# Kernel tuning notes

Hardware: AMD Instinct MI355X
Metric: run time of the kernel (lower is better)

Reference implementation:

```python
import jax, jax.numpy as jnp
import numpy as np

N_ROWS = 4096   # output dim (c_3)
N_COLS = 4096   # input dim (c_4)
NNZ = 4194304


def setup_inputs() -> dict:
    key = jax.random.key(0)
    k1, k2, k3, k4 = jax.random.split(key, 4)
    x = jax.random.normal(k1, (4, 2048, N_COLS), dtype=jnp.float32)
    values = jax.random.normal(k2, (NNZ,), dtype=jnp.float32)
    col_idx = jax.random.randint(k3, (NNZ,), 0, N_COLS, dtype=jnp.int32)
    row_ids = jnp.sort(jax.random.randint(k4, (NNZ,), 0, N_ROWS, dtype=jnp.int32))
    return {"x": x, "values": values, "col_idx": col_idx, "row_ids": row_ids}


def reference(x, values, col_idx, row_ids):
    # Faithful math of macko_spmv.multiply applied to every flattened row of x:
    #   out[..., r] = sum_k values[k] * x[..., col_idx[k]]  where row_ids[k] == r
    # Instead of N separate sparse matvecs (the original Python loop), scatter the
    # compressed weights into the dense matrix once and do a single batched GEMM.
    W = jnp.zeros((N_ROWS, N_COLS), dtype=values.dtype).at[row_ids, col_idx].add(values)
    return jnp.einsum('bsh,oh->bso', x, W)  # [B, S, N_ROWS]
```

## Files before the change

### kernel.cpp

```cpp
#include <hip/hip_runtime.h>


#define M_DIM 8192
#define K_DIM 4096
#define N_DIM 4096
#define NNZ   4194304
#define FXSCALE 1048576.0f
#define FXINV  (1.0f / 1048576.0f)

#define BKT 64
#define NTIL (K_DIM / BKT)
#define ABUF 16384

typedef __bf16 bf16x8 __attribute__((ext_vector_type(8)));
typedef float  floatx4 __attribute__((ext_vector_type(4)));
typedef unsigned short ushort8 __attribute__((ext_vector_type(8)));

__device__ __forceinline__ unsigned short f32_to_bf16(float f) {
  unsigned int u = __float_as_uint(f);
  u += 0x7FFFu + ((u >> 16) & 1u);
  return (unsigned short)(u >> 16);
}

__device__ __forceinline__ void async_copy16(const void* g, void* l) {
  __builtin_amdgcn_global_load_lds(
      (const __attribute__((address_space(1))) void*)g,
      (__attribute__((address_space(3))) void*)l,
      16, 0, 0);
}

__global__ void row_start_kernel(const int* __restrict__ rows,
                                 int* __restrict__ row_start) {
  int i = blockIdx.x * blockDim.x + threadIdx.x;
  if (i > NNZ) return;
  int cur  = (i < NNZ) ? rows[i] : N_DIM;
  int prev = (i > 0) ? rows[i - 1] : -1;
  for (int r = prev + 1; r <= cur; ++r) row_start[r] = i;
}

__global__ __launch_bounds__(256) void build_w_kernel(
    const float* __restrict__ vals,
    const int* __restrict__ cols,
    const int* __restrict__ row_start,
    unsigned short* __restrict__ Wb) {
  __shared__ int wrow[K_DIM];

  const int r = blockIdx.x;
  for (int i = threadIdx.x; i < K_DIM; i += 256) wrow[i] = 0;
  __syncthreads();

  const int start = row_start[r];
  const int end   = row_start[r + 1];
  for (int i = start + threadIdx.x; i < end; i += 256)
    atomicAdd(&wrow[cols[i]], (int)lrintf(vals[i] * FXSCALE));
  __syncthreads();

  ushort8* dst = (ushort8*)(Wb + (size_t)r * K_DIM);
  for (int i = threadIdx.x; i < K_DIM / 8; i += 256) {
    const int* s = &wrow[i * 8];
    ushort8 o;
#pragma unroll
    for (int j = 0; j < 8; j++) o[j] = f32_to_bf16((float)s[j] * FXINV);
    dst[i] = o;
  }
}

__global__ void cvt_kernel(const float4* __restrict__ in,
                           ushort4* __restrict__ out, int n4) {
  int i = blockIdx.x * blockDim.x + threadIdx.x;
  if (i < n4) {
    float4 v = in[i];
    ushort4 o;
    o.x = f32_to_bf16(v.x);
    o.y = f32_to_bf16(v.y);
    o.z = f32_to_bf16(v.z);
    o.w = f32_to_bf16(v.w);
    out[i] = o;
  }
}

#define BAR()   asm volatile("s_barrier" ::: "memory")
#define LGKM0() do { asm volatile("s_waitcnt lgkmcnt(0)" ::: "memory"); \
                     __builtin_amdgcn_sched_barrier(0); } while (0)
#define VMW6()  asm volatile("s_waitcnt vmcnt(6)" ::: "memory")
#define VMW0()  asm volatile("s_waitcnt vmcnt(0)" ::: "memory")

#define STAGEH(Gb_, Lb_, h_, kt_) do {                                          \
  async_copy16((Gb_) + (size_t)((h_)*128 +      srow) * K_DIM + (kt_),          \
               (Lb_) + (h_)*8192 +        tid * 8);                             \
  async_copy16((Gb_) + (size_t)((h_)*128 + 64 + srow) * K_DIM + (kt_),          \
               (Lb_) + (h_)*8192 + 4096 + tid * 8);                             \
} while (0)

#define RD_A(Ab_, mb_) do {                                                     \
  _Pragma("unroll")                                                             \
  for (int m_ = 0; m_ < 4; ++m_) {                                              \
    af[m_][0] = *(const bf16x8*)((Ab_) + offA[(mb_) + m_][0]);                  \
    af[m_][1] = *(const bf16x8*)((Ab_) + offA[(mb_) + m_][1]);                  \
  }                                                                             \
} while (0)

#define RD_B(Bb_, nb_) do {                                                     \
  _Pragma("unroll")                                                             \
  for (int n_ = 0; n_ < 2; ++n_) {                                              \
    bf[(nb_) + n_][0] = *(const bf16x8*)((Bb_) + offB[(nb_) + n_][0]);          \
    bf[(nb_) + n_][1] = *(const bf16x8*)((Bb_) + offB[(nb_) + n_][1]);          \
  }                                                                             \
} while (0)

#define MM(mb_, nb_) do {                                                       \
  __builtin_amdgcn_s_setprio(1);                                                \
  _Pragma("unroll")                                                             \
  for (int m_ = 0; m_ < 4; ++m_)                                                \
    _Pragma("unroll")                                                           \
    for (int n_ = 0; n_ < 2; ++n_) {                                            \
      acc[(mb_) + m_][(nb_) + n_] = __builtin_amdgcn_mfma_f32_16x16x32_bf16(    \
          af[m_][0], bf[(nb_) + n_][0], acc[(mb_) + m_][(nb_) + n_], 0, 0, 0);  \
      acc[(mb_) + m_][(nb_) + n_] = __builtin_amdgcn_mfma_f32_16x16x32_bf16(    \
          af[m_][1], bf[(nb_) + n_][1], acc[(mb_) + m_][(nb_) + n_], 0, 0, 0);  \
    }                                                                           \
  __builtin_amdgcn_s_setprio(0);                                                \
} while (0)

__global__ __launch_bounds__(512, 2) void gemm_bt(
    const unsigned short* __restrict__ A,
    const unsigned short* __restrict__ B,
    float* __restrict__ C) {
  __shared__ __attribute__((aligned(16))) unsigned short LDS[4][ABUF];

  const int tid  = threadIdx.x;
  const int wid  = tid >> 6;
  const int lane = tid & 63;
  const int quad = lane >> 4;
  const int l16  = lane & 15;
  const int mh   = wid >> 2;
  const int w32  = wid & 3;

  int wg = blockIdx.x;
  wg = (wg & 7) * 64 + (wg >> 3);
  const int n0 = (wg & 15) * 256;
  const int m0 = (wg >> 4) * 256;

  const int srow = tid >> 3;
  const int sblk = ((tid & 7) ^ ((tid >> 3) & 7)) * 8;
  const unsigned short* Abase = A + (size_t)m0 * K_DIM + sblk;
  const unsigned short* Bbase = B + (size_t)n0 * K_DIM + sblk;

  int offA[8][2], offB[4][2];
#pragma unroll
  for (int m = 0; m < 8; ++m) {
    const int r = (m < 4 ? mh * 64 + m * 16 : 128 + mh * 64 + (m - 4) * 16) + l16;
#pragma unroll
    for (int h = 0; h < 2; ++h)
      offA[m][h] = r * 64 + (((h * 4 + quad) ^ (r & 7)) * 8);
  }
#pragma unroll
  for (int n = 0; n < 4; ++n) {
    const int r = (n < 2 ? w32 * 32 + n * 16 : 128 + w32 * 32 + (n - 2) * 16) + l16;
#pragma unroll
    for (int h = 0; h < 2; ++h)
      offB[n][h] = r * 64 + (((h * 4 + quad) ^ (r & 7)) * 8);
  }

  floatx4 acc[8][4];
#pragma unroll
  for (int i = 0; i < 8; i++)
#pragma unroll
    for (int j = 0; j < 4; j++) acc[i][j] = (floatx4){0.f, 0.f, 0.f, 0.f};

  bf16x8 af[4][2], bf[4][2];

  unsigned short* A0L = &LDS[0][0];
  unsigned short* B0L = &LDS[1][0];
  unsigned short* A1L = &LDS[2][0];
  unsigned short* B1L = &LDS[3][0];

  STAGEH(Abase, A0L, 0, 0);
  STAGEH(Bbase, B0L, 0, 0);
  STAGEH(Abase, A0L, 1, 0);
  STAGEH(Bbase, B0L, 1, 0);
  STAGEH(Abase, A1L, 0, BKT);
  STAGEH(Bbase, B1L, 0, BKT);
  STAGEH(Abase, A1L, 1, BKT);
  VMW6();
  BAR();

  for (int i = 0; i < NTIL / 2 - 1; ++i) {
    const int ktE = (2 * i) * BKT;
    RD_A(A0L, 0); RD_B(B0L, 0);
    STAGEH(Bbase, B1L, 1, ktE + BKT);
    BAR(); LGKM0();
    MM(0, 0);
    BAR();
    RD_B(B0L, 2);
    STAGEH(Abase, A0L, 0, ktE + 2 * BKT);
    BAR(); LGKM0();
    MM(0, 2);
    BAR();
    RD_A(A0L, 4);
    STAGEH(Bbase, B0L, 0, ktE + 2 * BKT);
    BAR(); LGKM0();
    MM(4, 0);
    BAR();
    STAGEH(Abase, A0L, 1, ktE + 2 * BKT);
    BAR();
    MM(4, 2);
    VMW6();
    BAR();
    RD_A(A1L, 0); RD_B(B1L, 0);
    STAGEH(Bbase, B0L, 1, ktE + 2 * BKT);
    BAR(); LGKM0();
    MM(0, 0);
    BAR();
    RD_B(B1L, 2);
    STAGEH(Abase, A1L, 0, ktE + 3 * BKT);
    BAR(); LGKM0();
    MM(0, 2);
    BAR();
    RD_A(A1L, 4);
    STAGEH(Bbase, B1L, 0, ktE + 3 * BKT);
    BAR(); LGKM0();
    MM(4, 0);
    BAR();
    STAGEH(Abase, A1L, 1, ktE + 3 * BKT);
    BAR();
    MM(4, 2);
    VMW6();
    BAR();
  }

  {
    const int ktE = (NTIL - 2) * BKT;
    RD_A(A0L, 0); RD_B(B0L, 0);
    STAGEH(Bbase, B1L, 1, ktE + BKT);
    BAR(); LGKM0();
    MM(0, 0);
    BAR();
    RD_B(B0L, 2);
    BAR(); LGKM0();
    MM(0, 2);
    BAR();
    RD_A(A0L, 4);
    BAR(); LGKM0();
    MM(4, 0);
    BAR();
    MM(4, 2);
    VMW0();
    BAR();
    RD_A(A1L, 0); RD_B(B1L, 0);
    BAR(); LGKM0();
    MM(0, 0);
    BAR();
    RD_B(B1L, 2);
    BAR(); LGKM0();
    MM(0, 2);
    BAR();
    RD_A(A1L, 4);
    BAR(); LGKM0();
    MM(4, 0);
    BAR();
    MM(4, 2);
  }

#pragma unroll
  for (int m = 0; m < 8; m++) {
    const int mrow = (m < 4 ? mh * 64 + m * 16 : 128 + mh * 64 + (m - 4) * 16);
#pragma unroll
    for (int r = 0; r < 4; r++) {
      const int row = m0 + mrow + quad * 4 + r;
      float* Cp = C + (size_t)row * N_DIM + n0 + l16;
#pragma unroll
      for (int n = 0; n < 4; n++) {
        const int ncol = (n < 2 ? w32 * 32 + n * 16 : 128 + w32 * 32 + (n - 2) * 16);
        Cp[ncol] = acc[m][n][r];
      }
    }
  }
}

extern "C" void kernel_launch(void* const* d_in, const int* in_sizes, int n_in,
                              void* d_out, int out_size, void* d_ws, size_t ws_size,
                              hipStream_t stream) {
  const float* x       = (const float*)d_in[0];
  const float* values  = (const float*)d_in[1];
  const int*   col_idx = (const int*)d_in[2];
  const int*   row_ids = (const int*)d_in[3];
  float* out = (float*)d_out;

  unsigned short* Wb = (unsigned short*)d_ws;
  unsigned short* Xb = (unsigned short*)((char*)d_ws + ((size_t)32 << 20));
  int* row_start     = (int*)((char*)d_ws + ((size_t)96 << 20));

  const int x4 = M_DIM * K_DIM / 4;

  row_start_kernel<<<(NNZ + 256) / 256, 256, 0, stream>>>(row_ids, row_start);
  cvt_kernel<<<(x4 + 255) / 256, 256, 0, stream>>>((const float4*)x, (ushort4*)Xb, x4);
  build_w_kernel<<<N_DIM, 256, 0, stream>>>(values, col_idx, row_start, Wb);

  gemm_bt<<<dim3(512), 512, 0, stream>>>(Xb, Wb, out);
}
```

Before: 466.9 us.

## Fuse preprocessing kernels into one launch and precompute LDS read pointers

Replaces the row_start, conversion and weight-build kernels with a single preprocessing kernel. Each weight-row block finds its row range by binary search over the sorted row ids, and the remaining blocks convert x to bf16 with a grid-stride loop. This removes two launches, the row_start pass and its global buffer, and lets the conversion overlap with the weight build. In the GEMM, the per-fragment LDS offset arrays are replaced by eight base pointers plus compile-time constant offsets, which should lower register pressure and address arithmetic. The cost is two binary searches of about 22 steps per weight block.

```diff
diff --git a/kernel.cpp b/kernel.cpp
--- a/kernel.cpp
+++ b/kernel.cpp
@@ -11,6 +11,7 @@
 #define BKT 64
 #define NTIL (K_DIM / BKT)
 #define ABUF 16384
+#define CVT_BLOCKS 8192
 
 typedef __bf16 bf16x8 __attribute__((ext_vector_type(8)));
 typedef float  floatx4 __attribute__((ext_vector_type(4)));
@@ -29,53 +30,48 @@
       16, 0, 0);
 }
 
-__global__ void row_start_kernel(const int* __restrict__ rows,
-                                 int* __restrict__ row_start) {
-  int i = blockIdx.x * blockDim.x + threadIdx.x;
-  if (i > NNZ) return;
-  int cur  = (i < NNZ) ? rows[i] : N_DIM;
-  int prev = (i > 0) ? rows[i - 1] : -1;
-  for (int r = prev + 1; r <= cur; ++r) row_start[r] = i;
-}
-
-__global__ __launch_bounds__(256) void build_w_kernel(
-    const float* __restrict__ vals,
-    const int* __restrict__ cols,
-    const int* __restrict__ row_start,
-    unsigned short* __restrict__ Wb) {
-  __shared__ int wrow[K_DIM];
-
-  const int r = blockIdx.x;
-  for (int i = threadIdx.x; i < K_DIM; i += 256) wrow[i] = 0;
-  __syncthreads();
-
-  const int start = row_start[r];
-  const int end   = row_start[r + 1];
-  for (int i = start + threadIdx.x; i < end; i += 256)
-    atomicAdd(&wrow[cols[i]], (int)lrintf(vals[i] * FXSCALE));
-  __syncthreads();
-
-  ushort8* dst = (ushort8*)(Wb + (size_t)r * K_DIM);
-  for (int i = threadIdx.x; i < K_DIM / 8; i += 256) {
-    const int* s = &wrow[i * 8];
-    ushort8 o;
-#pragma unroll
-    for (int j = 0; j < 8; j++) o[j] = f32_to_bf16((float)s[j] * FXINV);
-    dst[i] = o;
-  }
-}
-
-__global__ void cvt_kernel(const float4* __restrict__ in,
-                           ushort4* __restrict__ out, int n4) {
-  int i = blockIdx.x * blockDim.x + threadIdx.x;
-  if (i < n4) {
-    float4 v = in[i];
-    ushort4 o;
-    o.x = f32_to_bf16(v.x);
-    o.y = f32_to_bf16(v.y);
-    o.z = f32_to_bf16(v.z);
-    o.w = f32_to_bf16(v.w);
-    out[i] = o;
+__global__ __launch_bounds__(256) void preproc_kernel(
+    const float4* __restrict__ x4in, ushort4* __restrict__ xbout,
+    const float* __restrict__ vals, const int* __restrict__ cols,
+    const int* __restrict__ rows, unsigned short* __restrict__ Wb) {
+  if (blockIdx.x < N_DIM) {
+    __shared__ int wrow[K_DIM];
+    const int r = blockIdx.x;
+
+    int lo = 0, hi = NNZ;
+    while (lo < hi) { int mid = (lo + hi) >> 1; if (rows[mid] < r) lo = mid + 1; else hi = mid; }
+    const int start = lo;
+    hi = NNZ;
+    while (lo < hi) { int mid = (lo + hi) >> 1; if (rows[mid] < r + 1) lo = mid + 1; else hi = mid; }
+    const int end = lo;
+
+    for (int i = threadIdx.x; i < K_DIM; i += 256) wrow[i] = 0;
+    __syncthreads();
+
+    for (int i = start + threadIdx.x; i < end; i += 256)
+      atomicAdd(&wrow[cols[i]], (int)lrintf(vals[i] * FXSCALE));
+    __syncthreads();
+
+    ushort8* dst = (ushort8*)(Wb + (size_t)r * K_DIM);
+    for (int i = threadIdx.x; i < K_DIM / 8; i += 256) {
+      const int* s = &wrow[i * 8];
+      ushort8 o;
+#pragma unroll
+      for (int j = 0; j < 8; j++) o[j] = f32_to_bf16((float)s[j] * FXINV);
+      dst[i] = o;
+    }
+  } else {
+    const int total = M_DIM * K_DIM / 4;
+    for (int i = (blockIdx.x - N_DIM) * 256 + threadIdx.x; i < total;
+         i += CVT_BLOCKS * 256) {
+      float4 v = x4in[i];
+      ushort4 o;
+      o.x = f32_to_bf16(v.x);
+      o.y = f32_to_bf16(v.y);
+      o.z = f32_to_bf16(v.z);
+      o.w = f32_to_bf16(v.w);
+      xbout[i] = o;
+    }
   }
 }
 
@@ -92,19 +88,22 @@
                (Lb_) + (h_)*8192 + 4096 + tid * 8);                             \
 } while (0)
 
-#define RD_A(Ab_, mb_) do {                                                     \
+#define ROFA(m_) ((m_) < 4 ? (m_) * 1024 : 8192 + ((m_) - 4) * 1024)
+#define ROFB(n_) ((n_) < 2 ? (n_) * 1024 : 8192 + ((n_) - 2) * 1024)
+
+#define RD_A(p0_, p1_, mb_) do {                                                \
   _Pragma("unroll")                                                             \
   for (int m_ = 0; m_ < 4; ++m_) {                                              \
-    af[m_][0] = *(const bf16x8*)((Ab_) + offA[(mb_) + m_][0]);                  \
-    af[m_][1] = *(const bf16x8*)((Ab_) + offA[(mb_) + m_][1]);                  \
+    af[m_][0] = *(const bf16x8*)((p0_) + ROFA((mb_) + m_));                     \
+    af[m_][1] = *(const bf16x8*)((p1_) + ROFA((mb_) + m_));                     \
   }                                                                             \
 } while (0)
 
-#define RD_B(Bb_, nb_) do {                                                     \
+#define RD_B(p0_, p1_, nb_) do {                                                \
   _Pragma("unroll")                                                             \
   for (int n_ = 0; n_ < 2; ++n_) {                                              \
-    bf[(nb_) + n_][0] = *(const bf16x8*)((Bb_) + offB[(nb_) + n_][0]);          \
-    bf[(nb_) + n_][1] = *(const bf16x8*)((Bb_) + offB[(nb_) + n_][1]);          \
+    bf[(nb_) + n_][0] = *(const bf16x8*)((p0_) + ROFB((nb_) + n_));             \
+    bf[(nb_) + n_][1] = *(const bf16x8*)((p1_) + ROFB((nb_) + n_));             \
   }                                                                             \
 } while (0)
 
@@ -146,21 +145,20 @@
   const unsigned short* Abase = A + (size_t)m0 * K_DIM + sblk;
   const unsigned short* Bbase = B + (size_t)n0 * K_DIM + sblk;
 
-  int offA[8][2], offB[4][2];
-#pragma unroll
-  for (int m = 0; m < 8; ++m) {
-    const int r = (m < 4 ? mh * 64 + m * 16 : 128 + mh * 64 + (m - 4) * 16) + l16;
-#pragma unroll
-    for (int h = 0; h < 2; ++h)
-      offA[m][h] = r * 64 + (((h * 4 + quad) ^ (r & 7)) * 8);
-  }
-#pragma unroll
-  for (int n = 0; n < 4; ++n) {
-    const int r = (n < 2 ? w32 * 32 + n * 16 : 128 + w32 * 32 + (n - 2) * 16) + l16;
-#pragma unroll
-    for (int h = 0; h < 2; ++h)
-      offB[n][h] = r * 64 + (((h * 4 + quad) ^ (r & 7)) * 8);
-  }
+  const int r7  = l16 & 7;
+  const int xt0 = (quad ^ r7) * 8;
+  const int xt1 = ((4 + quad) ^ r7) * 8;
+  const int aB  = (mh * 64 + l16) * 64;
+  const int bB  = (w32 * 32 + l16) * 64;
+
+  const unsigned short* pA0h0 = &LDS[0][0] + aB + xt0;
+  const unsigned short* pA0h1 = &LDS[0][0] + aB + xt1;
+  const unsigned short* pB0h0 = &LDS[1][0] + bB + xt0;
+  const unsigned short* pB0h1 = &LDS[1][0] + bB + xt1;
+  const unsigned short* pA1h0 = &LDS[2][0] + aB + xt0;
+  const unsigned short* pA1h1 = &LDS[2][0] + aB + xt1;
+  const unsigned short* pB1h0 = &LDS[3][0] + bB + xt0;
+  const unsigned short* pB1h1 = &LDS[3][0] + bB + xt1;
 
   floatx4 acc[8][4];
 #pragma unroll
@@ -187,17 +185,17 @@
 
   for (int i = 0; i < NTIL / 2 - 1; ++i) {
     const int ktE = (2 * i) * BKT;
-    RD_A(A0L, 0); RD_B(B0L, 0);
+    RD_A(pA0h0, pA0h1, 0); RD_B(pB0h0, pB0h1, 0);
     STAGEH(Bbase, B1L, 1, ktE + BKT);
     BAR(); LGKM0();
     MM(0, 0);
     BAR();
-    RD_B(B0L, 2);
+    RD_B(pB0h0, pB0h1, 2);
     STAGEH(Abase, A0L, 0, ktE + 2 * BKT);
     BAR(); LGKM0();
     MM(0, 2);
     BAR();
-    RD_A(A0L, 4);
+    RD_A(pA0h0, pA0h1, 4);
     STAGEH(Bbase, B0L, 0, ktE + 2 * BKT);
     BAR(); LGKM0();
     MM(4, 0);
@@ -207,17 +205,17 @@
     MM(4, 2);
     VMW6();
     BAR();
-    RD_A(A1L, 0); RD_B(B1L, 0);
+    RD_A(pA1h0, pA1h1, 0); RD_B(pB1h0, pB1h1, 0);
     STAGEH(Bbase, B0L, 1, ktE + 2 * BKT);
     BAR(); LGKM0();
     MM(0, 0);
     BAR();
-    RD_B(B1L, 2);
+    RD_B(pB1h0, pB1h1, 2);
     STAGEH(Abase, A1L, 0, ktE + 3 * BKT);
     BAR(); LGKM0();
     MM(0, 2);
     BAR();
-    RD_A(A1L, 4);
+    RD_A(pA1h0, pA1h1, 4);
     STAGEH(Bbase, B1L, 0, ktE + 3 * BKT);
     BAR(); LGKM0();
     MM(4, 0);
@@ -231,31 +229,31 @@
 
   {
     const int ktE = (NTIL - 2) * BKT;
-    RD_A(A0L, 0); RD_B(B0L, 0);
+    RD_A(pA0h0, pA0h1, 0); RD_B(pB0h0, pB0h1, 0);
     STAGEH(Bbase, B1L, 1, ktE + BKT);
     BAR(); LGKM0();
     MM(0, 0);
     BAR();
-    RD_B(B0L, 2);
-    BAR(); LGKM0();
-    MM(0, 2);
-    BAR();
-    RD_A(A0L, 4);
+    RD_B(pB0h0, pB0h1, 2);
+    BAR(); LGKM0();
+    MM(0, 2);
+    BAR();
+    RD_A(pA0h0, pA0h1, 4);
     BAR(); LGKM0();
     MM(4, 0);
     BAR();
     MM(4, 2);
     VMW0();
     BAR();
-    RD_A(A1L, 0); RD_B(B1L, 0);
-    BAR(); LGKM0();
-    MM(0, 0);
-    BAR();
-    RD_B(B1L, 2);
-    BAR(); LGKM0();
-    MM(0, 2);
-    BAR();
-    RD_A(A1L, 4);
+    RD_A(pA1h0, pA1h1, 0); RD_B(pB1h0, pB1h1, 0);
+    BAR(); LGKM0();
+    MM(0, 0);
+    BAR();
+    RD_B(pB1h0, pB1h1, 2);
+    BAR(); LGKM0();
+    MM(0, 2);
+    BAR();
+    RD_A(pA1h0, pA1h1, 4);
     BAR(); LGKM0();
     MM(4, 0);
     BAR();
@@ -289,13 +287,9 @@
 
   unsigned short* Wb = (unsigned short*)d_ws;
   unsigned short* Xb = (unsigned short*)((char*)d_ws + ((size_t)32 << 20));
-  int* row_start     = (int*)((char*)d_ws + ((size_t)96 << 20));
-
-  const int x4 = M_DIM * K_DIM / 4;
-
-  row_start_kernel<<<(NNZ + 256) / 256, 256, 0, stream>>>(row_ids, row_start);
-  cvt_kernel<<<(x4 + 255) / 256, 256, 0, stream>>>((const float4*)x, (ushort4*)Xb, x4);
-  build_w_kernel<<<N_DIM, 256, 0, stream>>>(values, col_idx, row_start, Wb);
+
+  preproc_kernel<<<N_DIM + CVT_BLOCKS, 256, 0, stream>>>(
+      (const float4*)x, (ushort4*)Xb, values, col_idx, row_ids, Wb);
 
   gemm_bt<<<dim3(512), 512, 0, stream>>>(Xb, Wb, out);
 }
```

New measurement: 481.5 us. +3.1%, slower.

## Switch GEMM inner loop from 16x16x32 to 32x32x16 bf16 MFMA tiles

Applied to the files above, without the earlier changes.

Replaces the 16x16x32 MFMA micro-tiles with 32x32x16 MFMA instructions, which reorganizes the accumulator layout (4x2 floatx16 instead of 8x4 floatx4), the LDS fragment reads and the epilogue store mapping. It also reorders the LDS buffers to A0,A1,B0,B1 so fragment pointers can be precomputed once and indexed by constant offsets instead of per-fragment offset tables. The larger MFMA shape is meant to cut LDS read traffic per FLOP and instruction-issue overhead. In exchange, the epilogue store pattern changes and register pressure shifts.

```diff
diff --git a/kernel.cpp b/kernel.cpp
--- a/kernel.cpp
+++ b/kernel.cpp
@@ -13,7 +13,7 @@
 #define ABUF 16384
 
 typedef __bf16 bf16x8 __attribute__((ext_vector_type(8)));
-typedef float  floatx4 __attribute__((ext_vector_type(4)));
+typedef float  floatx16 __attribute__((ext_vector_type(16)));
 typedef unsigned short ushort8 __attribute__((ext_vector_type(8)));
 
 __device__ __forceinline__ unsigned short f32_to_bf16(float f) {
@@ -92,33 +92,36 @@
                (Lb_) + (h_)*8192 + 4096 + tid * 8);                             \
 } while (0)
 
-#define RD_A(Ab_, mb_) do {                                                     \
-  _Pragma("unroll")                                                             \
-  for (int m_ = 0; m_ < 4; ++m_) {                                              \
-    af[m_][0] = *(const bf16x8*)((Ab_) + offA[(mb_) + m_][0]);                  \
-    af[m_][1] = *(const bf16x8*)((Ab_) + offA[(mb_) + m_][1]);                  \
-  }                                                                             \
+#define ROFA(m_) ((m_) == 0 ? 0 : (m_) == 1 ? 2048 : (m_) == 2 ? 8192 : 10240)
+#define ROFB(n_) ((n_) == 0 ? 0 : 8192)
+
+#define RD_A32(bi_, mb_) do {                                                   \
+  af[0][0] = *(const bf16x8*)(pAk0 + (bi_) + ROFA(mb_));                        \
+  af[0][1] = *(const bf16x8*)(pAk1 + (bi_) + ROFA(mb_));                        \
+  af[0][2] = *(const bf16x8*)(pAk2 + (bi_) + ROFA(mb_));                        \
+  af[0][3] = *(const bf16x8*)(pAk3 + (bi_) + ROFA(mb_));                        \
+  af[1][0] = *(const bf16x8*)(pAk0 + (bi_) + ROFA((mb_) + 1));                  \
+  af[1][1] = *(const bf16x8*)(pAk1 + (bi_) + ROFA((mb_) + 1));                  \
+  af[1][2] = *(const bf16x8*)(pAk2 + (bi_) + ROFA((mb_) + 1));                  \
+  af[1][3] = *(const bf16x8*)(pAk3 + (bi_) + ROFA((mb_) + 1));                  \
 } while (0)
 
-#define RD_B(Bb_, nb_) do {                                                     \
-  _Pragma("unroll")                                                             \
-  for (int n_ = 0; n_ < 2; ++n_) {                                              \
-    bf[(nb_) + n_][0] = *(const bf16x8*)((Bb_) + offB[(nb_) + n_][0]);          \
-    bf[(nb_) + n_][1] = *(const bf16x8*)((Bb_) + offB[(nb_) + n_][1]);          \
-  }                                                                             \
+#define RD_B32(bi_, nb_) do {                                                   \
+  bf[nb_][0] = *(const bf16x8*)(pBk0 + (bi_) + ROFB(nb_));                      \
+  bf[nb_][1] = *(const bf16x8*)(pBk1 + (bi_) + ROFB(nb_));                      \
+  bf[nb_][2] = *(const bf16x8*)(pBk2 + (bi_) + ROFB(nb_));                      \
+  bf[nb_][3] = *(const bf16x8*)(pBk3 + (bi_) + ROFB(nb_));                      \
 } while (0)
 
-#define MM(mb_, nb_) do {                                                       \
+#define MM32(mb_, nb_) do {                                                     \
   __builtin_amdgcn_s_setprio(1);                                                \
   _Pragma("unroll")                                                             \
-  for (int m_ = 0; m_ < 4; ++m_)                                                \
-    _Pragma("unroll")                                                           \
-    for (int n_ = 0; n_ < 2; ++n_) {                                            \
-      acc[(mb_) + m_][(nb_) + n_] = __builtin_amdgcn_mfma_f32_16x16x32_bf16(    \
-          af[m_][0], bf[(nb_) + n_][0], acc[(mb_) + m_][(nb_) + n_], 0, 0, 0);  \
-      acc[(mb_) + m_][(nb_) + n_] = __builtin_amdgcn_mfma_f32_16x16x32_bf16(    \
-          af[m_][1], bf[(nb_) + n_][1], acc[(mb_) + m_][(nb_) + n_], 0, 0, 0);  \
-    }                                                                           \
+  for (int ks_ = 0; ks_ < 4; ++ks_) {                                           \
+    acc[(mb_)][nb_] = __builtin_amdgcn_mfma_f32_32x32x16_bf16(                  \
+        af[0][ks_], bf[nb_][ks_], acc[(mb_)][nb_], 0, 0, 0);                    \
+    acc[(mb_) + 1][nb_] = __builtin_amdgcn_mfma_f32_32x32x16_bf16(              \
+        af[1][ks_], bf[nb_][ks_], acc[(mb_) + 1][nb_], 0, 0, 0);                \
+  }                                                                             \
   __builtin_amdgcn_s_setprio(0);                                                \
 } while (0)
 
@@ -131,8 +134,9 @@
   const int tid  = threadIdx.x;
   const int wid  = tid >> 6;
   const int lane = tid & 63;
-  const int quad = lane >> 4;
-  const int l16  = lane & 15;
+  const int l31  = lane & 31;
+  const int lhi  = lane >> 5;
+  const int l7   = lane & 7;
   const int mh   = wid >> 2;
   const int w32  = wid & 3;
 
@@ -146,33 +150,30 @@
   const unsigned short* Abase = A + (size_t)m0 * K_DIM + sblk;
   const unsigned short* Bbase = B + (size_t)n0 * K_DIM + sblk;
 
-  int offA[8][2], offB[4][2];
-#pragma unroll
-  for (int m = 0; m < 8; ++m) {
-    const int r = (m < 4 ? mh * 64 + m * 16 : 128 + mh * 64 + (m - 4) * 16) + l16;
-#pragma unroll
-    for (int h = 0; h < 2; ++h)
-      offA[m][h] = r * 64 + (((h * 4 + quad) ^ (r & 7)) * 8);
-  }
-#pragma unroll
-  for (int n = 0; n < 4; ++n) {
-    const int r = (n < 2 ? w32 * 32 + n * 16 : 128 + w32 * 32 + (n - 2) * 16) + l16;
-#pragma unroll
-    for (int h = 0; h < 2; ++h)
-      offB[n][h] = r * 64 + (((h * 4 + quad) ^ (r & 7)) * 8);
-  }
-
-  floatx4 acc[8][4];
-#pragma unroll
-  for (int i = 0; i < 8; i++)
-#pragma unroll
-    for (int j = 0; j < 4; j++) acc[i][j] = (floatx4){0.f, 0.f, 0.f, 0.f};
-
-  bf16x8 af[4][2], bf[4][2];
+  const int aB = (mh * 64 + l31) * 64;
+  const int bB = (w32 * 32 + l31) * 64;
+  const unsigned short* pAk0 = &LDS[0][0] + aB + (((0 + lhi) ^ l7) * 8);
+  const unsigned short* pAk1 = &LDS[0][0] + aB + (((2 + lhi) ^ l7) * 8);
+  const unsigned short* pAk2 = &LDS[0][0] + aB + (((4 + lhi) ^ l7) * 8);
+  const unsigned short* pAk3 = &LDS[0][0] + aB + (((6 + lhi) ^ l7) * 8);
+  const unsigned short* pBk0 = &LDS[2][0] + bB + (((0 + lhi) ^ l7) * 8);
+  const unsigned short* pBk1 = &LDS[2][0] + bB + (((2 + lhi) ^ l7) * 8);
+  const unsigned short* pBk2 = &LDS[2][0] + bB + (((4 + lhi) ^ l7) * 8);
+  const unsigned short* pBk3 = &LDS[2][0] + bB + (((6 + lhi) ^ l7) * 8);
+
+  floatx16 acc[4][2];
+#pragma unroll
+  for (int i = 0; i < 4; i++)
+#pragma unroll
+    for (int j = 0; j < 2; j++)
+#pragma unroll
+      for (int e = 0; e < 16; e++) acc[i][j][e] = 0.f;
+
+  bf16x8 af[2][4], bf[2][4];
 
   unsigned short* A0L = &LDS[0][0];
-  unsigned short* B0L = &LDS[1][0];
-  unsigned short* A1L = &LDS[2][0];
+  unsigned short* A1L = &LDS[1][0];
+  unsigned short* B0L = &LDS[2][0];
   unsigned short* B1L = &LDS[3][0];
 
   STAGEH(Abase, A0L, 0, 0);
@@ -187,92 +188,92 @@
 
   for (int i = 0; i < NTIL / 2 - 1; ++i) {
     const int ktE = (2 * i) * BKT;
-    RD_A(A0L, 0); RD_B(B0L, 0);
+    RD_A32(0, 0); RD_B32(0, 0);
     STAGEH(Bbase, B1L, 1, ktE + BKT);
     BAR(); LGKM0();
-    MM(0, 0);
-    BAR();
-    RD_B(B0L, 2);
+    MM32(0, 0);
+    BAR();
+    RD_B32(0, 1);
     STAGEH(Abase, A0L, 0, ktE + 2 * BKT);
     BAR(); LGKM0();
-    MM(0, 2);
-    BAR();
-    RD_A(A0L, 4);
+    MM32(0, 1);
+    BAR();
+    RD_A32(0, 2);
     STAGEH(Bbase, B0L, 0, ktE + 2 * BKT);
     BAR(); LGKM0();
-    MM(4, 0);
+    MM32(2, 0);
     BAR();
     STAGEH(Abase, A0L, 1, ktE + 2 * BKT);
     BAR();
-    MM(4, 2);
+    MM32(2, 1);
     VMW6();
     BAR();
-    RD_A(A1L, 0); RD_B(B1L, 0);
+    RD_A32(16384, 0); RD_B32(16384, 0);
     STAGEH(Bbase, B0L, 1, ktE + 2 * BKT);
     BAR(); LGKM0();
-    MM(0, 0);
-    BAR();
-    RD_B(B1L, 2);
+    MM32(0, 0);
+    BAR();
+    RD_B32(16384, 1);
     STAGEH(Abase, A1L, 0, ktE + 3 * BKT);
     BAR(); LGKM0();
-    MM(0, 2);
-    BAR();
-    RD_A(A1L, 4);
+    MM32(0, 1);
+    BAR();
+    RD_A32(16384, 2);
     STAGEH(Bbase, B1L, 0, ktE + 3 * BKT);
     BAR(); LGKM0();
-    MM(4, 0);
+    MM32(2, 0);
     BAR();
     STAGEH(Abase, A1L, 1, ktE + 3 * BKT);
     BAR();
-    MM(4, 2);
+    MM32(2, 1);
     VMW6();
     BAR();
   }
 
   {
     const int ktE = (NTIL - 2) * BKT;
-    RD_A(A0L, 0); RD_B(B0L, 0);
+    RD_A32(0, 0); RD_B32(0, 0);
     STAGEH(Bbase, B1L, 1, ktE + BKT);
     BAR(); LGKM0();
-    MM(0, 0);
-    BAR();
-    RD_B(B0L, 2);
-    BAR(); LGKM0();
-    MM(0, 2);
-    BAR();
-    RD_A(A0L, 4);
-    BAR(); LGKM0();
-    MM(4, 0);
-    BAR();
-    MM(4, 2);
+    MM32(0, 0);
+    BAR();
+    RD_B32(0, 1);
+    BAR(); LGKM0();
+    MM32(0, 1);
+    BAR();
+    RD_A32(0, 2);
+    BAR(); LGKM0();
+    MM32(2, 0);
+    BAR();
+    MM32(2, 1);
     VMW0();
     BAR();
-    RD_A(A1L, 0); RD_B(B1L, 0);
-    BAR(); LGKM0();
-    MM(0, 0);
-    BAR();
-    RD_B(B1L, 2);
-    BAR(); LGKM0();
-    MM(0, 2);
-    BAR();
-    RD_A(A1L, 4);
-    BAR(); LGKM0();
-    MM(4, 0);
-    BAR();
-    MM(4, 2);
-  }
-
-#pragma unroll
-  for (int m = 0; m < 8; m++) {
-    const int mrow = (m < 4 ? mh * 64 + m * 16 : 128 + mh * 64 + (m - 4) * 16);
-#pragma unroll
-    for (int r = 0; r < 4; r++) {
-      const int row = m0 + mrow + quad * 4 + r;
-      float* Cp = C + (size_t)row * N_DIM + n0 + l16;
-#pragma unroll
-      for (int n = 0; n < 4; n++) {
-        const int ncol = (n < 2 ? w32 * 32 + n * 16 : 128 + w32 * 32 + (n - 2) * 16);
-        Cp[ncol] = acc[m][n][r];
+    RD_A32(16384, 0); RD_B32(16384, 0);
+    BAR(); LGKM0();
+    MM32(0, 0);
+    BAR();
+    RD_B32(16384, 1);
+    BAR(); LGKM0();
+    MM32(0, 1);
+    BAR();
+    RD_A32(16384, 2);
+    BAR(); LGKM0();
+    MM32(2, 0);
+    BAR();
+    MM32(2, 1);
+  }
+
+#pragma unroll
+  for (int m = 0; m < 4; m++) {
+    const int arow = (m < 2 ? mh * 64 + m * 32 : 128 + mh * 64 + (m - 2) * 32);
+#pragma unroll
+    for (int rg = 0; rg < 4; rg++) {
+#pragma unroll
+      for (int rr = 0; rr < 4; rr++) {
+        const int row = m0 + arow + rr + rg * 8 + lhi * 4;
+        float* Cp = C + (size_t)row * N_DIM + n0 + l31;
+        Cp[w32 * 32]       = acc[m][0][rg * 4 + rr];
+        Cp[128 + w32 * 32] = acc[m][1][rg * 4 + rr];
       }
     }
   }
```

New measurement: 705.0 us. +51.0%, slower.
